# Optimization experiments

Measured on AMD Instinct MI355X. Metric: run time of the kernel, lower is better.

## Reference

```python
import jax, jax.numpy as jnp
import numpy as np

B, T, I, H, NCLS = 256, 784, 1, 110, 10


def setup_inputs() -> dict:
    key = jax.random.key(0)
    ks = jax.random.split(key, 10)
    s = 1.0 / np.sqrt(H)
    u = lambda k, shape: jax.random.uniform(k, shape, jnp.float32, -s, s)
    return {
        "x": jax.random.normal(ks[0], (B, T, I), jnp.float32),
        "W_ih": u(ks[1], (4 * H, I)),
        "W_hh": u(ks[2], (4 * H, H)),
        "b": u(ks[3], (4 * H,)),
        "W_p": u(ks[4], (1, H)),     # skip-gate readout of cell state
        "b_p": jnp.ones((1,), jnp.float32),  # bias init ~1 -> start by updating
        "h0": u(ks[5], (H,)),        # learned initial hidden (learn_init=True)
        "c0": u(ks[6], (H,)),        # learned initial cell
        "W_fc": u(ks[7], (NCLS, H)),
        "b_fc": u(ks[8], (NCLS,)),
    }


def _st_round(u):
    # straight-through binarization: round in fwd, identity grad in bwd
    return u + jax.lax.stop_gradient(jnp.round(u) - u)


def reference(x, W_ih, W_hh, b, W_p, b_p, h0, c0, W_fc, b_fc):
    Bsz = x.shape[0]
    Hh = h0.shape[0]
    xT = jnp.transpose(x, (1, 0, 2))  # [T, B, I] (the permute in Net.forward)
    h = jnp.broadcast_to(h0, (Bsz, Hh))
    c = jnp.broadcast_to(c0, (Bsz, Hh))
    u0 = jnp.ones((Bsz, 1), x.dtype)  # first step always updates

    def step(carry, xt):
        h, c, u = carry
        ub = _st_round(u)                                  # binary update gate [B,1]
        gates = xt @ W_ih.T + h @ W_hh.T + b               # [B, 4H]
        i, f, g, o = jnp.split(gates, 4, axis=-1)
        i = jax.nn.sigmoid(i)
        f = jax.nn.sigmoid(f)
        o = jax.nn.sigmoid(o)
        g = jnp.tanh(g)
        c_new = f * c + i * g
        h_new = o * jnp.tanh(c_new)
        c_n = ub * c_new + (1.0 - ub) * c                  # skip: keep old state
        h_n = ub * h_new + (1.0 - ub) * h
        du = jax.nn.sigmoid(c_n @ W_p.T + b_p)             # delta-u from cell [B,1]
        u_n = ub * du + (1.0 - ub) * (u + jnp.minimum(du, 1.0 - u))
        return (h_n, c_n, u_n), (h_n, ub)

    (h_last, _, _), (hs, ubs) = jax.lax.scan(step, (h, c, u0), xT)
    out = hs[-1] @ W_fc.T + b_fc                           # fc on last timestep
    total_u = jnp.sum(ubs)                                 # total number of updates
    return out, total_u[None]
```

## Files before the change

kernel.cpp:

```cpp
#include <hip/hip_runtime.h>
#include <stdint.h>


#define T784 784
#define H110 110
#define NT   512
#define NCLS 10
#define LOG2E 1.44269504088896340736f
#define WQS  (0.09535f / 127.0f)

__device__ __forceinline__ float frcp(float x)  { return __builtin_amdgcn_rcpf(x); }
__device__ __forceinline__ float fexp2(float x) { return __builtin_amdgcn_exp2f(x); }

__device__ __forceinline__ float add_q1(float v) {
    float d; asm("v_add_f32_dpp %0, %1, %1 quad_perm:[1,0,3,2] row_mask:0xf bank_mask:0xf bound_ctrl:0"
                 : "=v"(d) : "v"(v)); return d;
}
__device__ __forceinline__ float add_q2(float v) {
    float d; asm("v_add_f32_dpp %0, %1, %1 quad_perm:[2,3,0,1] row_mask:0xf bank_mask:0xf bound_ctrl:0"
                 : "=v"(d) : "v"(v)); return d;
}
__device__ __forceinline__ float add_hm(float v) {
    float d; asm("v_add_f32_dpp %0, %1, %1 row_half_mirror row_mask:0xf bank_mask:0xf bound_ctrl:0"
                 : "=v"(d) : "v"(v)); return d;
}
__device__ __forceinline__ float add_rm(float v) {
    float d; asm("v_add_f32_dpp %0, %1, %1 row_mirror row_mask:0xf bank_mask:0xf bound_ctrl:0"
                 : "=v"(d) : "v"(v)); return d;
}
__device__ __forceinline__ float add_b15(float v) {
    float d; asm("v_add_f32_dpp %0, %1, %1 row_bcast:15 row_mask:0xf bank_mask:0xf bound_ctrl:0"
                 : "=v"(d) : "v"(v)); return d;
}
__device__ __forceinline__ float add_b31(float v) {
    float d; asm("v_add_f32_dpp %0, %1, %1 row_bcast:31 row_mask:0xf bank_mask:0xf bound_ctrl:0"
                 : "=v"(d) : "v"(v)); return d;
}
template <int L>
__device__ __forceinline__ float qbcast(float v) {
    float d;
    if (L == 0) asm("v_mov_b32_dpp %0, %1 quad_perm:[0,0,0,0] row_mask:0xf bank_mask:0xf bound_ctrl:0" : "=v"(d) : "v"(v));
    if (L == 1) asm("v_mov_b32_dpp %0, %1 quad_perm:[1,1,1,1] row_mask:0xf bank_mask:0xf bound_ctrl:0" : "=v"(d) : "v"(v));
    if (L == 2) asm("v_mov_b32_dpp %0, %1 quad_perm:[2,2,2,2] row_mask:0xf bank_mask:0xf bound_ctrl:0" : "=v"(d) : "v"(v));
    if (L == 3) asm("v_mov_b32_dpp %0, %1 quad_perm:[3,3,3,3] row_mask:0xf bank_mask:0xf bound_ctrl:0" : "=v"(d) : "v"(v));
    return d;
}

__device__ __forceinline__ int qpack(float f0, float f1, float f2, float f3) {
    const int q0 = (int)rintf(f0) & 0xFF;
    const int q1 = (int)rintf(f1) & 0xFF;
    const int q2 = (int)rintf(f2) & 0xFF;
    const int q3 = (int)rintf(f3) & 0xFF;
    return q0 | (q1 << 8) | (q2 << 16) | (q3 << 24);
}

__global__ __launch_bounds__(NT, 2)
void skiplstm_kernel(const float* __restrict__ x,
                     const float* __restrict__ W_ih,
                     const float* __restrict__ W_hh,
                     const float* __restrict__ b,
                     const float* __restrict__ W_p,
                     const float* __restrict__ b_p,
                     const float* __restrict__ h0,
                     const float* __restrict__ c0,
                     const float* __restrict__ W_fc,
                     const float* __restrict__ b_fc,
                     float* __restrict__ out)
{
    __shared__ int   s_h8[2][32];
    __shared__ float s_pbuf[256];
    __shared__ float s_x[T784];

    const int tid  = threadIdx.x;
    const int bb   = blockIdx.x;
    const int q    = tid >> 2;
    const int j    = tid & 3;
    const bool qact = (q < H110);

    const float qinv = 1.0f / WQS;
    const float gfac = (j == 2) ? (-2.0f * LOG2E) : (-LOG2E);
    const int   row  = j * H110 + q;
    const float bv = qact ? b[row]    * gfac : 0.0f;
    const float wv = qact ? W_ih[row] * gfac : 0.0f;
    const float scj = (WQS / 127.0f) * gfac;
    int w[28];
    {
        const float* rp = W_hh + row * H110;
        #pragma unroll
        for (int d = 0; d < 28; ++d) {
            float f[4];
            #pragma unroll
            for (int e = 0; e < 4; ++e) {
                const int k = 4 * d + e;
                f[e] = (qact && k < H110) ? rp[k] * qinv : 0.0f;
            }
            w[d] = qpack(f[0], f[1], f[2], f[3]);
        }
    }

    float creg = qact ? c0[q] : 0.0f;
    float hreg = qact ? h0[q] : 0.0f;
    const float wpn = qact ? (-LOG2E) * W_p[q] : 0.0f;
    const float bpn = (-LOG2E) * b_p[0];

    const float mulc = (j == 2) ? 2.0f : 1.0f;
    const float addc = (j == 2) ? -1.0f : 0.0f;

    for (int i = tid; i < 64;   i += NT) ((int*)s_h8)[i] = 0;
    for (int i = tid; i < 256;  i += NT) s_pbuf[i] = 0.0f;
    for (int i = tid; i < T784; i += NT) s_x[i] = x[bb * T784 + i];
    __syncthreads();
    if (tid < H110)
        ((int8_t*)s_h8[0])[tid] = (int8_t)__float2int_rn(h0[tid] * 127.0f);
    __syncthreads();

    float u_prev = 1.0f;
    int   cnt    = 0;

    auto step = [&](const int* hb, int* hn,
                    const float* pp, float* pn, int t, bool first) {
        const int lane = tid & 63;
        const float p0 = pp[lane], p1 = pp[lane + 64];
        const float xt = s_x[t];
        int h8[28];
        #pragma unroll
        for (int d = 0; d < 7; ++d) {
            const int4 v = ((const int4*)hb)[d];
            h8[4 * d + 0] = v.x; h8[4 * d + 1] = v.y;
            h8[4 * d + 2] = v.z; h8[4 * d + 3] = v.w;
        }

        int ia0 = 0, ia1 = 0, ia2 = 0, ia3 = 0;
        #pragma unroll
        for (int d = 0; d < 7; ++d) {
            ia0 = __builtin_amdgcn_sdot4(h8[4 * d + 0], w[4 * d + 0], ia0, false);
            ia1 = __builtin_amdgcn_sdot4(h8[4 * d + 1], w[4 * d + 1], ia1, false);
            ia2 = __builtin_amdgcn_sdot4(h8[4 * d + 2], w[4 * d + 2], ia2, false);
            ia3 = __builtin_amdgcn_sdot4(h8[4 * d + 3], w[4 * d + 3], ia3, false);
        }
        const int ia = (ia0 + ia1) + (ia2 + ia3);
        const float asel = fmaf((float)ia, scj, fmaf(xt, wv, bv));

        float u_now;
        if (first) {
            u_now = 1.0f;
        } else {
            float v = p0 + p1;
            v = add_q1(v); v = add_q2(v); v = add_hm(v);
            v = add_rm(v); v = add_b15(v); v = add_b31(v);
            const float tot = __int_as_float(
                __builtin_amdgcn_readlane(__float_as_int(v), 63));
            const float du = frcp(1.0f + fexp2(tot + bpn));
            u_now = (u_prev > 0.5f) ? du
                                    : (u_prev + fminf(du, 1.0f - u_prev));
        }
        const bool up = u_now > 0.5f;
        cnt += up ? 1 : 0;
        u_prev = u_now;

        const float av = fmaf(mulc, frcp(1.0f + fexp2(asel)), addc);
        const float gi = qbcast<0>(av);
        const float gf = qbcast<1>(av);
        const float gg = qbcast<2>(av);
        const float go = qbcast<3>(av);

        const float cn = fmaf(gf, creg, gi * gg);
        const float th = fmaf(2.0f, frcp(1.0f + fexp2(cn * (-2.0f * LOG2E))), -1.0f);
        const float hn_ = go * th;
        creg = up ? cn : creg;
        hreg = up ? hn_ : hreg;
        if (qact && j == 0) {
            ((int8_t*)hn)[q] = (int8_t)__float2int_rn(hreg * 127.0f);
            pn[q] = creg * wpn;
        }
        __syncthreads();
    };

    int* const h0b = s_h8[0];
    int* const h1b = s_h8[1];
    float* const p0b = s_pbuf;
    float* const p1b = s_pbuf + 128;

    step(h0b, h1b, p0b, p1b, 0, true);
    step(h1b, h0b, p1b, p0b, 1, false);
    step(h0b, h1b, p0b, p1b, 2, false);
    step(h1b, h0b, p1b, p0b, 3, false);
    for (int t = 4; t < T784; t += 4) {
        step(h0b, h1b, p0b, p1b, t,     false);
        step(h1b, h0b, p1b, p0b, t + 1, false);
        step(h0b, h1b, p0b, p1b, t + 2, false);
        step(h1b, h0b, p1b, p0b, t + 3, false);
    }

    if (qact && j == 0) s_pbuf[q] = hreg;
    __syncthreads();
    if (tid < NCLS) {
        float acc = b_fc[tid];
        for (int k = 0; k < H110; ++k)
            acc = fmaf(s_pbuf[k], W_fc[tid * H110 + k], acc);
        out[bb * NCLS + tid] = acc;
    }
    if (tid == 0)
        atomicAdd(out + 256 * NCLS, (float)cnt);
}

__global__ void zero_tail_kernel(float* out) {
    if (threadIdx.x == 0) out[256 * NCLS] = 0.0f;
}

extern "C" void kernel_launch(void* const* d_in, const int* in_sizes, int n_in,
                              void* d_out, int out_size, void* d_ws, size_t ws_size,
                              hipStream_t stream) {
    const float* x    = (const float*)d_in[0];
    const float* W_ih = (const float*)d_in[1];
    const float* W_hh = (const float*)d_in[2];
    const float* b    = (const float*)d_in[3];
    const float* W_p  = (const float*)d_in[4];
    const float* b_p  = (const float*)d_in[5];
    const float* h0   = (const float*)d_in[6];
    const float* c0   = (const float*)d_in[7];
    const float* W_fc = (const float*)d_in[8];
    const float* b_fc = (const float*)d_in[9];
    float* out = (float*)d_out;

    zero_tail_kernel<<<1, 64, 0, stream>>>(out);
    skiplstm_kernel<<<256, NT, 0, stream>>>(x, W_ih, W_hh, b, W_p, b_p,
                                            h0, c0, W_fc, b_fc, out);
}
```

Baseline: 467.0 us.

## Split recurrent dot product across two lanes per gate and double block size

Each gate row's int8 dot product over the hidden state is now split in half across two lanes, so eight lanes serve one hidden unit instead of four, and the block grows to 1024 threads. The two partial sums are combined with a row_half_mirror DPP exchange; the gate index is mirrored so paired lanes hold the same gate. The aim is a shorter serial sdot4 chain on each recurrent step. In exchange the per-step barrier now spans twice as many waves, an extra cross-lane op sits on the critical path, and the tighter launch bounds may constrain registers.

```diff
diff --git a/kernel.cpp b/kernel.cpp
--- a/kernel.cpp
+++ b/kernel.cpp
@@ -4,7 +4,7 @@
 
 #define T784 784
 #define H110 110
-#define NT   512
+#define NT   1024
 #define NCLS 10
 #define LOG2E 1.44269504088896340736f
 #define WQS  (0.09535f / 127.0f)
@@ -35,6 +35,10 @@
 __device__ __forceinline__ float add_b31(float v) {
     float d; asm("v_add_f32_dpp %0, %1, %1 row_bcast:31 row_mask:0xf bank_mask:0xf bound_ctrl:0"
                  : "=v"(d) : "v"(v)); return d;
+}
+__device__ __forceinline__ int xch_hm_i32(int v) {
+    int d; asm("v_mov_b32_dpp %0, %1 row_half_mirror row_mask:0xf bank_mask:0xf bound_ctrl:0"
+               : "=v"(d) : "v"(v)); return d;
 }
 template <int L>
 __device__ __forceinline__ float qbcast(float v) {
@@ -54,7 +58,7 @@
     return q0 | (q1 << 8) | (q2 << 16) | (q3 << 24);
 }
 
-__global__ __launch_bounds__(NT, 2)
+__global__ __launch_bounds__(NT, 4)
 void skiplstm_kernel(const float* __restrict__ x,
                      const float* __restrict__ W_ih,
                      const float* __restrict__ W_hh,
@@ -67,44 +71,46 @@
                      const float* __restrict__ b_fc,
                      float* __restrict__ out)
 {
-    __shared__ int   s_h8[2][32];
+    __shared__ __align__(16) int s_h8[2][32];
     __shared__ float s_pbuf[256];
     __shared__ float s_x[T784];
 
     const int tid  = threadIdx.x;
     const int bb   = blockIdx.x;
-    const int q    = tid >> 2;
-    const int j    = tid & 3;
-    const bool qact = (q < H110);
+    const int o    = tid >> 3;
+    const int j    = tid & 7;
+    const int g    = (j < 4) ? j : 7 - j;
+    const int kh   = j >> 2;
+    const bool qact = (o < H110);
 
     const float qinv = 1.0f / WQS;
-    const float gfac = (j == 2) ? (-2.0f * LOG2E) : (-LOG2E);
-    const int   row  = j * H110 + q;
+    const float gfac = (g == 2) ? (-2.0f * LOG2E) : (-LOG2E);
+    const int   row  = g * H110 + o;
     const float bv = qact ? b[row]    * gfac : 0.0f;
     const float wv = qact ? W_ih[row] * gfac : 0.0f;
     const float scj = (WQS / 127.0f) * gfac;
-    int w[28];
+    int w[16];
     {
         const float* rp = W_hh + row * H110;
         #pragma unroll
-        for (int d = 0; d < 28; ++d) {
+        for (int d = 0; d < 16; ++d) {
             float f[4];
             #pragma unroll
             for (int e = 0; e < 4; ++e) {
-                const int k = 4 * d + e;
+                const int k = 64 * kh + 4 * d + e;
                 f[e] = (qact && k < H110) ? rp[k] * qinv : 0.0f;
             }
             w[d] = qpack(f[0], f[1], f[2], f[3]);
         }
     }
 
-    float creg = qact ? c0[q] : 0.0f;
-    float hreg = qact ? h0[q] : 0.0f;
-    const float wpn = qact ? (-LOG2E) * W_p[q] : 0.0f;
-    const float bpn = (-LOG2E) * b_p[0];
-
-    const float mulc = (j == 2) ? 2.0f : 1.0f;
-    const float addc = (j == 2) ? -1.0f : 0.0f;
+    float creg = qact ? c0[o] : 0.0f;
+    float hreg = qact ? h0[o] : 0.0f;
+    const float wpn = qact ? (-LOG2E) * W_p[o] : 0.0f;
+    const float bpn  = (-LOG2E) * b_p[0];
+
+    const float mulc = (g == 2) ? 2.0f : 1.0f;
+    const float addc = (g == 2) ? -1.0f : 0.0f;
 
     for (int i = tid; i < 64;   i += NT) ((int*)s_h8)[i] = 0;
     for (int i = tid; i < 256;  i += NT) s_pbuf[i] = 0.0f;
@@ -122,23 +128,24 @@
         const int lane = tid & 63;
         const float p0 = pp[lane], p1 = pp[lane + 64];
         const float xt = s_x[t];
-        int h8[28];
+        int h8[16];
         #pragma unroll
-        for (int d = 0; d < 7; ++d) {
-            const int4 v = ((const int4*)hb)[d];
+        for (int d = 0; d < 4; ++d) {
+            const int4 v = ((const int4*)hb)[4 * kh + d];
             h8[4 * d + 0] = v.x; h8[4 * d + 1] = v.y;
             h8[4 * d + 2] = v.z; h8[4 * d + 3] = v.w;
         }
 
         int ia0 = 0, ia1 = 0, ia2 = 0, ia3 = 0;
         #pragma unroll
-        for (int d = 0; d < 7; ++d) {
+        for (int d = 0; d < 4; ++d) {
             ia0 = __builtin_amdgcn_sdot4(h8[4 * d + 0], w[4 * d + 0], ia0, false);
             ia1 = __builtin_amdgcn_sdot4(h8[4 * d + 1], w[4 * d + 1], ia1, false);
             ia2 = __builtin_amdgcn_sdot4(h8[4 * d + 2], w[4 * d + 2], ia2, false);
             ia3 = __builtin_amdgcn_sdot4(h8[4 * d + 3], w[4 * d + 3], ia3, false);
         }
-        const int ia = (ia0 + ia1) + (ia2 + ia3);
+        const int iah = (ia0 + ia1) + (ia2 + ia3);
+        const int ia  = iah + xch_hm_i32(iah);
         const float asel = fmaf((float)ia, scj, fmaf(xt, wv, bv));
 
         float u_now;
@@ -170,8 +177,8 @@
         creg = up ? cn : creg;
         hreg = up ? hn_ : hreg;
         if (qact && j == 0) {
-            ((int8_t*)hn)[q] = (int8_t)__float2int_rn(hreg * 127.0f);
-            pn[q] = creg * wpn;
+            ((int8_t*)hn)[o] = (int8_t)__float2int_rn(hreg * 127.0f);
+            pn[o] = creg * wpn;
         }
         __syncthreads();
     };
@@ -192,7 +199,7 @@
         step(h1b, h0b, p1b, p0b, t + 3, false);
     }
 
-    if (qact && j == 0) s_pbuf[q] = hreg;
+    if (qact && j == 0) s_pbuf[o] = hreg;
     __syncthreads();
     if (tid < NCLS) {
         float acc = b_fc[tid];
```

Result: slower. 601.0 us (+28.7%).

## Compute recurrent int8 matvec with MFMA instead of per-thread sdot4

Applied to the files above, without the earlier changes.

Replaces the per-thread 28-element sdot4 dot product over quantized W_hh with int8 MFMA 16x16x64 instructions, where each wave holds its 16 gate rows as packed A fragments and the broadcast hidden vector is the B operand. Results are written from one column of lanes into a per-wave LDS scratch and read back per lane to form the gate pre-activation. This cuts the dependent dot-product instruction chain on the serial recurrence and frees many weight registers. In exchange it adds an LDS store/load round trip and an explicit wait within each step, and it relies on a particular MFMA operand and output lane layout being correct.

```diff
diff --git a/kernel.cpp b/kernel.cpp
--- a/kernel.cpp
+++ b/kernel.cpp
@@ -8,6 +8,8 @@
 #define NCLS 10
 #define LOG2E 1.44269504088896340736f
 #define WQS  (0.09535f / 127.0f)
+
+typedef int v4i __attribute__((ext_vector_type(4)));
 
 __device__ __forceinline__ float frcp(float x)  { return __builtin_amdgcn_rcpf(x); }
 __device__ __forceinline__ float fexp2(float x) { return __builtin_amdgcn_exp2f(x); }
@@ -67,36 +69,49 @@
                      const float* __restrict__ b_fc,
                      float* __restrict__ out)
 {
-    __shared__ int   s_h8[2][32];
+    __shared__ __align__(16) int s_h8[2][32];
     __shared__ float s_pbuf[256];
     __shared__ float s_x[T784];
+    __shared__ __align__(16) int s_gate[8 * 64];
 
     const int tid  = threadIdx.x;
     const int bb   = blockIdx.x;
+    const int lane = tid & 63;
+    const int wid  = tid >> 6;
     const int q    = tid >> 2;
     const int j    = tid & 3;
     const bool qact = (q < H110);
 
     const float qinv = 1.0f / WQS;
+    const int r16  = lane & 15;
+    const int grp  = lane >> 4;
+    const int ga   = r16 & 3;
+    v4i aw[4][2];
+    #pragma unroll
+    for (int t = 0; t < 4; ++t) {
+        const int u = 16 * wid + 4 * t + (r16 >> 2);
+        const bool ua = (u < H110);
+        const float* rp = W_hh + (ga * H110 + u) * H110;
+        #pragma unroll
+        for (int kk = 0; kk < 2; ++kk) {
+            #pragma unroll
+            for (int d = 0; d < 4; ++d) {
+                float f[4];
+                #pragma unroll
+                for (int e = 0; e < 4; ++e) {
+                    const int k = kk * 64 + grp * 16 + 4 * d + e;
+                    f[e] = (ua && k < H110) ? rp[k] * qinv : 0.0f;
+                }
+                aw[t][kk][d] = qpack(f[0], f[1], f[2], f[3]);
+            }
+        }
+    }
+
     const float gfac = (j == 2) ? (-2.0f * LOG2E) : (-LOG2E);
     const int   row  = j * H110 + q;
     const float bv = qact ? b[row]    * gfac : 0.0f;
     const float wv = qact ? W_ih[row] * gfac : 0.0f;
     const float scj = (WQS / 127.0f) * gfac;
-    int w[28];
-    {
-        const float* rp = W_hh + row * H110;
-        #pragma unroll
-        for (int d = 0; d < 28; ++d) {
-            float f[4];
-            #pragma unroll
-            for (int e = 0; e < 4; ++e) {
-                const int k = 4 * d + e;
-                f[e] = (qact && k < H110) ? rp[k] * qinv : 0.0f;
-            }
-            w[d] = qpack(f[0], f[1], f[2], f[3]);
-        }
-    }
 
     float creg = qact ? c0[q] : 0.0f;
     float hreg = qact ? h0[q] : 0.0f;
@@ -116,30 +131,32 @@
 
     float u_prev = 1.0f;
     int   cnt    = 0;
+    int* const gsc = s_gate + wid * 64;
 
     auto step = [&](const int* hb, int* hn,
                     const float* pp, float* pn, int t, bool first) {
-        const int lane = tid & 63;
         const float p0 = pp[lane], p1 = pp[lane + 64];
         const float xt = s_x[t];
-        int h8[28];
-        #pragma unroll
-        for (int d = 0; d < 7; ++d) {
-            const int4 v = ((const int4*)hb)[d];
-            h8[4 * d + 0] = v.x; h8[4 * d + 1] = v.y;
-            h8[4 * d + 2] = v.z; h8[4 * d + 3] = v.w;
-        }
-
-        int ia0 = 0, ia1 = 0, ia2 = 0, ia3 = 0;
-        #pragma unroll
-        for (int d = 0; d < 7; ++d) {
-            ia0 = __builtin_amdgcn_sdot4(h8[4 * d + 0], w[4 * d + 0], ia0, false);
-            ia1 = __builtin_amdgcn_sdot4(h8[4 * d + 1], w[4 * d + 1], ia1, false);
-            ia2 = __builtin_amdgcn_sdot4(h8[4 * d + 2], w[4 * d + 2], ia2, false);
-            ia3 = __builtin_amdgcn_sdot4(h8[4 * d + 3], w[4 * d + 3], ia3, false);
-        }
-        const int ia = (ia0 + ia1) + (ia2 + ia3);
-        const float asel = fmaf((float)ia, scj, fmaf(xt, wv, bv));
+        const v4i bh0 = ((const v4i*)hb)[grp];
+        const v4i bh1 = ((const v4i*)hb)[grp + 4];
+
+        v4i acc0 = {0, 0, 0, 0}, acc1 = {0, 0, 0, 0};
+        v4i acc2 = {0, 0, 0, 0}, acc3 = {0, 0, 0, 0};
+        acc0 = __builtin_amdgcn_mfma_i32_16x16x64_i8(aw[0][0], bh0, acc0, 0, 0, 0);
+        acc1 = __builtin_amdgcn_mfma_i32_16x16x64_i8(aw[1][0], bh0, acc1, 0, 0, 0);
+        acc2 = __builtin_amdgcn_mfma_i32_16x16x64_i8(aw[2][0], bh0, acc2, 0, 0, 0);
+        acc3 = __builtin_amdgcn_mfma_i32_16x16x64_i8(aw[3][0], bh0, acc3, 0, 0, 0);
+        acc0 = __builtin_amdgcn_mfma_i32_16x16x64_i8(aw[0][1], bh1, acc0, 0, 0, 0);
+        acc1 = __builtin_amdgcn_mfma_i32_16x16x64_i8(aw[1][1], bh1, acc1, 0, 0, 0);
+        acc2 = __builtin_amdgcn_mfma_i32_16x16x64_i8(aw[2][1], bh1, acc2, 0, 0, 0);
+        acc3 = __builtin_amdgcn_mfma_i32_16x16x64_i8(aw[3][1], bh1, acc3, 0, 0, 0);
+
+        if ((lane & 15) == 0) {
+            ((v4i*)gsc)[grp]      = acc0;
+            ((v4i*)gsc)[grp + 4]  = acc1;
+            ((v4i*)gsc)[grp + 8]  = acc2;
+            ((v4i*)gsc)[grp + 12] = acc3;
+        }
 
         float u_now;
         if (first) {
@@ -157,6 +174,11 @@
         const bool up = u_now > 0.5f;
         cnt += up ? 1 : 0;
         u_prev = u_now;
+
+        asm volatile("s_waitcnt lgkmcnt(0)" ::: "memory");
+        __builtin_amdgcn_sched_barrier(0);
+        const int ia = gsc[lane];
+        const float asel = fmaf((float)ia, scj, fmaf(xt, wv, bv));
 
         const float av = fmaf(mulc, frcp(1.0f + fexp2(asel)), addc);
         const float gi = qbcast<0>(av);
```

After: 527.6 us. 1.13x slower.
